# Performance work log

Hardware: AMD Instinct MI355X
Metric: run time of the kernel (lower is better)

Reference implementation:

```python
import jax, jax.numpy as jnp
import numpy as np

NUM_ENT = 14541
NUM_REL = 474
D = 400
B = 32
N_CAND = 14505


def setup_inputs() -> dict:
    key = jax.random.key(0)
    k0, k1, k2, k4, k5 = jax.random.split(key, 5)
    return {
        "arg0_1": jax.random.normal(k0, (NUM_ENT, D), dtype=jnp.float32),   # entity embeddings
        "arg1_1": jax.random.normal(k1, (NUM_REL, D), dtype=jnp.float32),   # relation centers
        "arg2_1": jax.random.uniform(k2, (NUM_REL, D), dtype=jnp.float32),  # relation offsets (box widths)
        "arg3_1": jnp.ones((1,), dtype=jnp.float32),                        # margin gamma
        "arg4_1": jax.random.randint(k4, (B, 2), 0, NUM_REL),               # (head_id, rel_id) pairs
        "arg5_1": jax.random.randint(k5, (4, N_CAND), 0, NUM_ENT),          # candidate entity ids (row 0 used)
    }


def reference(arg0_1, arg1_1, arg2_1, arg3_1, arg4_1, arg5_1):
    # Gather heads / relation params
    head = arg0_1[arg4_1[:, 0]]            # [B, D]
    rel_c = arg1_1[arg4_1[:, 1]]           # [B, D]
    rel_o = arg2_1[arg4_1[:, 1]]           # [B, D]

    query = (head + rel_c)[:, None, :]     # [B, 1, D] box center
    offset = rel_o[:, None, :]             # [B, 1, D] box width

    # Candidate tail embeddings: only row 0 of arg5_1 is used in the graph
    cand = arg0_1[arg5_1[0].reshape(-1)][None, :, :]  # [1, N_CAND, D]

    d = jnp.abs(cand - query)                           # [B, N_CAND, D]
    dist_outside = jax.nn.relu(d - offset).sum(-1)      # [B, N_CAND]
    dist_inside = jnp.abs(jnp.minimum(d, offset)).sum(-1)

    return arg3_1 - dist_outside - 0.02 * dist_inside   # [B, N_CAND]
```

## Files before the change

kernel.cpp:

```cpp
#include <hip/hip_runtime.h>

#define DIM     400
#define NENT    14541
#define B       32
#define NCAND   14505
#define NROUND  3627
#define NSTRIPS 256
#define THREADS 256
#define DROWS   14508
#define CVTN    (DROWS * 50)
#define CVTBLK  ((CVTN + THREADS - 1) / THREADS)

typedef __attribute__((ext_vector_type(2))) _Float16 half2_t;

static __device__ __forceinline__ half2_t bch(unsigned u) {
    return __builtin_bit_cast(half2_t, u);
}
static __device__ __forceinline__ half2_t habs2(half2_t x) {
    unsigned u = __builtin_bit_cast(unsigned, x) & 0x7fff7fffu;
    return __builtin_bit_cast(half2_t, u);
}
static __device__ __forceinline__ unsigned pkh(float x, float y) {
    half2_t h;
    h.x = (_Float16)x;
    h.y = (_Float16)y;
    return __builtin_bit_cast(unsigned, h);
}
static __device__ __forceinline__ float dot2acc(half2_t m, float s) {
#if __has_builtin(__builtin_amdgcn_fdot2)
    const half2_t ones = {(_Float16)1.f, (_Float16)1.f};
    return __builtin_amdgcn_fdot2(m, ones, s, false);
#else
    return s + (float)m.x + (float)m.y;
#endif
}

__global__ void setup_kernel(const float* __restrict__ ent,
                             const float* __restrict__ relc,
                             const float* __restrict__ relo,
                             const float* __restrict__ onev,
                             const int*   __restrict__ pairs,
                             const int*   __restrict__ cidx,
                             uint4* __restrict__ dense16,
                             _Float16* __restrict__ q16,
                             _Float16* __restrict__ o16,
                             float* __restrict__ baseg) {
    const int blk = blockIdx.x;
    const int tid = threadIdx.x;
    if (blk < CVTBLK) {
        int i = blk * THREADS + tid;
        if (i >= CVTN) return;
        int row = i / 50;
        int col = i - row * 50;
        int n  = row < NCAND ? row : NCAND - 1;
        int ci = cidx[n];
        const float4* s4 = (const float4*)(ent + (size_t)ci * DIM) + col * 2;
        float4 a = s4[0], c = s4[1];
        uint4 d;
        d.x = pkh(a.x, a.y);
        d.y = pkh(a.z, a.w);
        d.z = pkh(c.x, c.y);
        d.w = pkh(c.z, c.w);
        dense16[i] = d;
    } else {
        const int b = blk - CVTBLK;
        const int h = pairs[2 * b + 0];
        const int r = pairs[2 * b + 1];
        float so = 0.f;
        for (int i = tid; i < DIM; i += THREADS) {
            float qv = ent[(size_t)h * DIM + i] + relc[(size_t)r * DIM + i];
            float ov = relo[(size_t)r * DIM + i];
            q16[(size_t)b * DIM + i] = (_Float16)qv;
            o16[(size_t)b * DIM + i] = (_Float16)(0.98f * ov);
            so += ov;
        }
        __shared__ float sred[4];
        for (int off = 32; off; off >>= 1) so += __shfl_down(so, off);
        if ((tid & 63) == 0) sred[tid >> 6] = so;
        __syncthreads();
        if (tid == 0)
            baseg[b] = onev[0] + 0.98f * (sred[0] + sred[1] + sred[2] + sred[3]);
    }
}

__global__ __launch_bounds__(THREADS, 2)
void score_f16(const uint4* __restrict__ dense16,
               const uint4* __restrict__ q16,
               const uint4* __restrict__ o16,
               const float* __restrict__ baseg,
               float* __restrict__ out) {
    const int fid  = blockIdx.x;
    const int xcd  = fid & 7;
    const int rest = fid >> 3;
    const int beta = rest & 3;
    const int tc   = rest >> 2;
    const int strip = xcd + 8 * tc;

    const int r0 = strip * 14 + (strip < 43 ? strip : 43);
    const int r1 = r0 + 14 + (strip < 43 ? 1 : 0);

    const int tid  = threadIdx.x;
    const int wid  = tid >> 6;
    const int lane = tid & 63;
    const int u    = lane & 15;
    const int g    = lane >> 4;
    const int b0   = __builtin_amdgcn_readfirstlane(8 * beta + 2 * wid);
    const int b1   = b0 + 1;

    const uint4* qa = q16 + (size_t)b0 * 50;
    const uint4* oa = o16 + (size_t)b0 * 50;
    const uint4* qc = q16 + (size_t)b1 * 50;
    const uint4* oc = o16 + (size_t)b1 * 50;

    uint4 q0[4], o0[4], q1[4], o1[4];
    q0[0] = qa[u]; q0[1] = qa[u + 16]; q0[2] = qa[u + 32];
    o0[0] = oa[u]; o0[1] = oa[u + 16]; o0[2] = oa[u + 32];
    q1[0] = qc[u]; q1[1] = qc[u + 16]; q1[2] = qc[u + 32];
    o1[0] = oc[u]; o1[1] = oc[u + 16]; o1[2] = oc[u + 32];
    q0[3] = q0[0]; o0[3] = o0[0]; q1[3] = q1[0]; o1[3] = o1[0];
    if (u < 2) {
        q0[3] = qa[48 + u]; o0[3] = oa[48 + u];
        q1[3] = qc[48 + u]; o1[3] = oc[48 + u];
    }
    const float base0 = baseg[b0];
    const float base1 = baseg[b1];

    const half2_t K002 = {(_Float16)0.02f, (_Float16)0.02f};

#define PAIR(cu, qu, ou, SS)                                    \
    {                                                           \
        half2_t cc_ = bch(cu), qq_ = bch(qu), oo_ = bch(ou);    \
        half2_t dd_ = cc_ - qq_;                                \
        half2_t aa_ = habs2(dd_);                               \
        half2_t ee_ = aa_ * K002 + oo_;                         \
        half2_t mm_ = __builtin_elementwise_max(aa_, ee_);      \
        SS = dot2acc(mm_, SS);                                  \
    }
#define PROC(C, Q, O, SA, SB)                                   \
    PAIR(C.x, Q.x, O.x, SA) PAIR(C.y, Q.y, O.y, SB)             \
    PAIR(C.z, Q.z, O.z, SA) PAIR(C.w, Q.w, O.w, SB)

    for (int rr = r0; rr < r1; rr += 2) {
        const int rA = rr;
        const int rB = (rr + 1 < r1) ? rr + 1 : rr;
        const uint4* pA = dense16 + (size_t)(4 * rA + g) * 50;
        const uint4* pB = dense16 + (size_t)(4 * rB + g) * 50;

        uint4 av0 = pA[u], av1 = pA[u + 16], av2 = pA[u + 32];
        uint4 bv0 = pB[u], bv1 = pB[u + 16], bv2 = pB[u + 32];
        uint4 av3, bv3;
        if (u < 2) { av3 = pA[48 + u]; bv3 = pB[48 + u]; }

        float sA00 = 0.f, sA01 = 0.f, sA10 = 0.f, sA11 = 0.f;
        float sB00 = 0.f, sB01 = 0.f, sB10 = 0.f, sB11 = 0.f;

        PROC(av0, q0[0], o0[0], sA00, sA01)
        PROC(av1, q0[1], o0[1], sA00, sA01)
        PROC(av2, q0[2], o0[2], sA00, sA01)
        PROC(av0, q1[0], o1[0], sA10, sA11)
        PROC(av1, q1[1], o1[1], sA10, sA11)
        PROC(av2, q1[2], o1[2], sA10, sA11)
        if (u < 2) {
            PROC(av3, q0[3], o0[3], sA00, sA01)
            PROC(av3, q1[3], o1[3], sA10, sA11)
        }
        PROC(bv0, q0[0], o0[0], sB00, sB01)
        PROC(bv1, q0[1], o0[1], sB00, sB01)
        PROC(bv2, q0[2], o0[2], sB00, sB01)
        PROC(bv0, q1[0], o1[0], sB10, sB11)
        PROC(bv1, q1[1], o1[1], sB10, sB11)
        PROC(bv2, q1[2], o1[2], sB10, sB11)
        if (u < 2) {
            PROC(bv3, q0[3], o0[3], sB00, sB01)
            PROC(bv3, q1[3], o1[3], sB10, sB11)
        }

        float sA0 = sA00 + sA01;
        float sA1 = sA10 + sA11;
        float sB0 = sB00 + sB01;
        float sB1 = sB10 + sB11;
        sA0 += __shfl_xor(sA0, 1); sA1 += __shfl_xor(sA1, 1);
        sB0 += __shfl_xor(sB0, 1); sB1 += __shfl_xor(sB1, 1);
        sA0 += __shfl_xor(sA0, 2); sA1 += __shfl_xor(sA1, 2);
        sB0 += __shfl_xor(sB0, 2); sB1 += __shfl_xor(sB1, 2);
        sA0 += __shfl_xor(sA0, 4); sA1 += __shfl_xor(sA1, 4);
        sB0 += __shfl_xor(sB0, 4); sB1 += __shfl_xor(sB1, 4);
        sA0 += __shfl_xor(sA0, 8); sA1 += __shfl_xor(sA1, 8);
        sB0 += __shfl_xor(sB0, 8); sB1 += __shfl_xor(sB1, 8);

        if (u == 0) {
            const int candA = 4 * rA + g;
            const int candB = 4 * rB + g;
            if (candA < NCAND) {
                out[(size_t)b0 * NCAND + candA] = base0 - sA0;
                out[(size_t)b1 * NCAND + candA] = base1 - sA1;
            }
            if (rB != rA && candB < NCAND) {
                out[(size_t)b0 * NCAND + candB] = base0 - sB0;
                out[(size_t)b1 * NCAND + candB] = base1 - sB1;
            }
        }
    }
#undef PROC
#undef PAIR
}

__global__ __launch_bounds__(THREADS, 2)
void score_f32(const float* __restrict__ ent,
               const float* __restrict__ relc,
               const float* __restrict__ relo,
               const float* __restrict__ onev,
               const int*   __restrict__ pairs,
               const int*   __restrict__ cidx,
               float* __restrict__ out) {
    const int fid  = blockIdx.x;
    const int xcd  = fid & 7;
    const int rest = fid >> 3;
    const int bq   = rest & 7;
    const int tc   = rest >> 3;
    const int t    = xcd + 8 * tc;

    const int tid  = threadIdx.x;
    const int lane = tid & 63;
    const int u    = lane & 15;
    const int g    = lane >> 4;
    const int b    = __builtin_amdgcn_readfirstlane(bq * 4 + (tid >> 6));

    const int hd = pairs[b * 2 + 0];
    const int rl = pairs[b * 2 + 1];
    const float4* hb = (const float4*)(ent  + (size_t)hd * DIM) + u;
    const float4* cb = (const float4*)(relc + (size_t)rl * DIM) + u;
    const float4* ob = (const float4*)(relo + (size_t)rl * DIM) + u;

    float4 q[7], o[7];
    float oa = 0.f;
#pragma unroll
    for (int k = 0; k < 6; ++k) {
        float4 h = hb[16 * k], c = cb[16 * k];
        q[k] = make_float4(h.x + c.x, h.y + c.y, h.z + c.z, h.w + c.w);
        o[k] = ob[16 * k];
        oa += o[k].x + o[k].y + o[k].z + o[k].w;
    }
    if (u < 4) {
        float4 h = hb[96], c = cb[96];
        q[6] = make_float4(h.x + c.x, h.y + c.y, h.z + c.z, h.w + c.w);
        o[6] = ob[96];
        oa += o[6].x + o[6].y + o[6].z + o[6].w;
    }
    oa += __shfl_xor(oa, 1);
    oa += __shfl_xor(oa, 2);
    oa += __shfl_xor(oa, 4);
    oa += __shfl_xor(oa, 8);
    const float base = onev[0] + 0.98f * oa;

    const float4* entu = (const float4*)ent + u;

#define E(vc, vq, vo, AM, AD)                     \
        {                                         \
            float d_ = (vc) - (vq);               \
            AM += fmaxf(fabsf(d_), (vo));         \
            AD += fabsf(d_);                      \
        }
#define F4(k, AM, AD)                             \
        E(cbuf[k].x, q[k].x, o[k].x, AM, AD)      \
        E(cbuf[k].y, q[k].y, o[k].y, AM, AD)      \
        E(cbuf[k].z, q[k].z, o[k].z, AM, AD)      \
        E(cbuf[k].w, q[k].w, o[k].w, AM, AD)

    for (int rr = t; rr < NROUND; rr += NSTRIPS) {
        const int cand = 4 * rr + g;
        const int ci   = cidx[cand < NCAND ? cand : NCAND - 1];
        const float4* p = entu + (size_t)ci * 100;

        float4 cbuf[7];
#pragma unroll
        for (int k = 0; k < 6; ++k) cbuf[k] = p[16 * k];
        if (u < 4) cbuf[6] = p[96];

        float am0 = 0.f, ad0 = 0.f, am1 = 0.f, ad1 = 0.f;
        F4(0, am0, ad0) F4(1, am1, ad1)
        F4(2, am0, ad0) F4(3, am1, ad1)
        F4(4, am0, ad0) F4(5, am1, ad1)
        if (u < 4) { F4(6, am0, ad0) }

        float s_ = fmaf(-0.98f, am0 + am1, -0.02f * (ad0 + ad1));
        s_ += __shfl_xor(s_, 1);
        s_ += __shfl_xor(s_, 2);
        s_ += __shfl_xor(s_, 4);
        s_ += __shfl_xor(s_, 8);

        if (u == 0 && cand < NCAND)
            out[(size_t)b * NCAND + cand] = base + s_;
    }
#undef F4
#undef E
}

extern "C" void kernel_launch(void* const* d_in, const int* in_sizes, int n_in,
                              void* d_out, int out_size, void* d_ws, size_t ws_size,
                              hipStream_t stream) {
    const float* ent   = (const float*)d_in[0];
    const float* relc  = (const float*)d_in[1];
    const float* relo  = (const float*)d_in[2];
    const float* onev  = (const float*)d_in[3];
    const int*   pairs = (const int*)d_in[4];
    const int*   cidx  = (const int*)d_in[5];
    float*       out   = (float*)d_out;

    const size_t denB = (size_t)DROWS * DIM * 2;
    const size_t qB   = (size_t)B * DIM * 2;
    const size_t need = denB + 2 * qB + B * sizeof(float);

    if (ws_size >= need) {
        unsigned char* w = (unsigned char*)d_ws;
        uint4*    dense16 = (uint4*)w;
        _Float16* q16     = (_Float16*)(w + denB);
        _Float16* o16     = (_Float16*)(w + denB + qB);
        float*    baseg   = (float*)(w + denB + 2 * qB);

        setup_kernel<<<CVTBLK + B, THREADS, 0, stream>>>(
            ent, relc, relo, onev, pairs, cidx, dense16, q16, o16, baseg);
        score_f16<<<8 * 4 * 32, THREADS, 0, stream>>>(
            dense16, (const uint4*)q16, (const uint4*)o16, baseg, out);
    } else {
        score_f32<<<8 * 8 * 32, THREADS, 0, stream>>>(
            ent, relc, relo, onev, pairs, cidx, out);
    }
}
```

Baseline: 39.84 us.

## Compute query/offset in score kernel and assign one batch row per wave

```diff
diff --git a/kernel.cpp b/kernel.cpp
--- a/kernel.cpp
+++ b/kernel.cpp
@@ -5,7 +5,6 @@
 #define B       32
 #define NCAND   14505
 #define NROUND  3627
-#define NSTRIPS 256
 #define THREADS 256
 #define DROWS   14508
 #define CVTN    (DROWS * 50)
@@ -36,64 +35,37 @@
 }
 
 __global__ void setup_kernel(const float* __restrict__ ent,
-                             const float* __restrict__ relc,
-                             const float* __restrict__ relo,
-                             const float* __restrict__ onev,
-                             const int*   __restrict__ pairs,
                              const int*   __restrict__ cidx,
-                             uint4* __restrict__ dense16,
-                             _Float16* __restrict__ q16,
-                             _Float16* __restrict__ o16,
-                             float* __restrict__ baseg) {
-    const int blk = blockIdx.x;
-    const int tid = threadIdx.x;
-    if (blk < CVTBLK) {
-        int i = blk * THREADS + tid;
-        if (i >= CVTN) return;
-        int row = i / 50;
-        int col = i - row * 50;
-        int n  = row < NCAND ? row : NCAND - 1;
-        int ci = cidx[n];
-        const float4* s4 = (const float4*)(ent + (size_t)ci * DIM) + col * 2;
-        float4 a = s4[0], c = s4[1];
-        uint4 d;
-        d.x = pkh(a.x, a.y);
-        d.y = pkh(a.z, a.w);
-        d.z = pkh(c.x, c.y);
-        d.w = pkh(c.z, c.w);
-        dense16[i] = d;
-    } else {
-        const int b = blk - CVTBLK;
-        const int h = pairs[2 * b + 0];
-        const int r = pairs[2 * b + 1];
-        float so = 0.f;
-        for (int i = tid; i < DIM; i += THREADS) {
-            float qv = ent[(size_t)h * DIM + i] + relc[(size_t)r * DIM + i];
-            float ov = relo[(size_t)r * DIM + i];
-            q16[(size_t)b * DIM + i] = (_Float16)qv;
-            o16[(size_t)b * DIM + i] = (_Float16)(0.98f * ov);
-            so += ov;
-        }
-        __shared__ float sred[4];
-        for (int off = 32; off; off >>= 1) so += __shfl_down(so, off);
-        if ((tid & 63) == 0) sred[tid >> 6] = so;
-        __syncthreads();
-        if (tid == 0)
-            baseg[b] = onev[0] + 0.98f * (sred[0] + sred[1] + sred[2] + sred[3]);
-    }
+                             uint4* __restrict__ dense16) {
+    int i = blockIdx.x * THREADS + threadIdx.x;
+    if (i >= CVTN) return;
+    int row = i / 50;
+    int col = i - row * 50;
+    int n  = row < NCAND ? row : NCAND - 1;
+    int ci = cidx[n];
+    const float4* s4 = (const float4*)(ent + (size_t)ci * DIM) + col * 2;
+    float4 a = s4[0], c = s4[1];
+    uint4 d;
+    d.x = pkh(a.x, a.y);
+    d.y = pkh(a.z, a.w);
+    d.z = pkh(c.x, c.y);
+    d.w = pkh(c.z, c.w);
+    dense16[i] = d;
 }
 
 __global__ __launch_bounds__(THREADS, 2)
 void score_f16(const uint4* __restrict__ dense16,
-               const uint4* __restrict__ q16,
-               const uint4* __restrict__ o16,
-               const float* __restrict__ baseg,
+               const float* __restrict__ ent,
+               const float* __restrict__ relc,
+               const float* __restrict__ relo,
+               const float* __restrict__ onev,
+               const int*   __restrict__ pairs,
                float* __restrict__ out) {
     const int fid  = blockIdx.x;
     const int xcd  = fid & 7;
     const int rest = fid >> 3;
-    const int beta = rest & 3;
-    const int tc   = rest >> 2;
+    const int bq   = rest & 7;
+    const int tc   = rest >> 3;
     const int strip = xcd + 8 * tc;
 
     const int r0 = strip * 14 + (strip < 43 ? strip : 43);
@@ -104,26 +76,53 @@
     const int lane = tid & 63;
     const int u    = lane & 15;
     const int g    = lane >> 4;
-    const int b0   = __builtin_amdgcn_readfirstlane(8 * beta + 2 * wid);
-    const int b1   = b0 + 1;
-
-    const uint4* qa = q16 + (size_t)b0 * 50;
-    const uint4* oa = o16 + (size_t)b0 * 50;
-    const uint4* qc = q16 + (size_t)b1 * 50;
-    const uint4* oc = o16 + (size_t)b1 * 50;
-
-    uint4 q0[4], o0[4], q1[4], o1[4];
-    q0[0] = qa[u]; q0[1] = qa[u + 16]; q0[2] = qa[u + 32];
-    o0[0] = oa[u]; o0[1] = oa[u + 16]; o0[2] = oa[u + 32];
-    q1[0] = qc[u]; q1[1] = qc[u + 16]; q1[2] = qc[u + 32];
-    o1[0] = oc[u]; o1[1] = oc[u + 16]; o1[2] = oc[u + 32];
-    q0[3] = q0[0]; o0[3] = o0[0]; q1[3] = q1[0]; o1[3] = o1[0];
+    const int b    = __builtin_amdgcn_readfirstlane(4 * bq + wid);
+
+    const int hd = pairs[2 * b + 0];
+    const int rl = pairs[2 * b + 1];
+    const float4* hp = (const float4*)(ent  + (size_t)hd * DIM);
+    const float4* cp = (const float4*)(relc + (size_t)rl * DIM);
+    const float4* op = (const float4*)(relo + (size_t)rl * DIM);
+
+    uint4 q[4], o[4];
+    float oa = 0.f;
+#pragma unroll
+    for (int k = 0; k < 3; ++k) {
+        const int f = 2 * u + 32 * k;
+        float4 h0 = hp[f], h1 = hp[f + 1];
+        float4 c0 = cp[f], c1 = cp[f + 1];
+        float4 v0 = op[f], v1 = op[f + 1];
+        q[k].x = pkh(h0.x + c0.x, h0.y + c0.y);
+        q[k].y = pkh(h0.z + c0.z, h0.w + c0.w);
+        q[k].z = pkh(h1.x + c1.x, h1.y + c1.y);
+        q[k].w = pkh(h1.z + c1.z, h1.w + c1.w);
+        o[k].x = pkh(0.98f * v0.x, 0.98f * v0.y);
+        o[k].y = pkh(0.98f * v0.z, 0.98f * v0.w);
+        o[k].z = pkh(0.98f * v1.x, 0.98f * v1.y);
+        o[k].w = pkh(0.98f * v1.z, 0.98f * v1.w);
+        oa += v0.x + v0.y + v0.z + v0.w + v1.x + v1.y + v1.z + v1.w;
+    }
+    q[3] = q[0]; o[3] = o[0];
     if (u < 2) {
-        q0[3] = qa[48 + u]; o0[3] = oa[48 + u];
-        q1[3] = qc[48 + u]; o1[3] = oc[48 + u];
-    }
-    const float base0 = baseg[b0];
-    const float base1 = baseg[b1];
+        const int f = 96 + 2 * u;
+        float4 h0 = hp[f], h1 = hp[f + 1];
+        float4 c0 = cp[f], c1 = cp[f + 1];
+        float4 v0 = op[f], v1 = op[f + 1];
+        q[3].x = pkh(h0.x + c0.x, h0.y + c0.y);
+        q[3].y = pkh(h0.z + c0.z, h0.w + c0.w);
+        q[3].z = pkh(h1.x + c1.x, h1.y + c1.y);
+        q[3].w = pkh(h1.z + c1.z, h1.w + c1.w);
+        o[3].x = pkh(0.98f * v0.x, 0.98f * v0.y);
+        o[3].y = pkh(0.98f * v0.z, 0.98f * v0.w);
+        o[3].z = pkh(0.98f * v1.x, 0.98f * v1.y);
+        o[3].w = pkh(0.98f * v1.z, 0.98f * v1.w);
+        oa += v0.x + v0.y + v0.z + v0.w + v1.x + v1.y + v1.z + v1.w;
+    }
+    oa += __shfl_xor(oa, 1);
+    oa += __shfl_xor(oa, 2);
+    oa += __shfl_xor(oa, 4);
+    oa += __shfl_xor(oa, 8);
+    const float base = onev[0] + 0.98f * oa;
 
     const half2_t K002 = {(_Float16)0.02f, (_Float16)0.02f};
 
@@ -151,54 +150,30 @@
         uint4 av3, bv3;
         if (u < 2) { av3 = pA[48 + u]; bv3 = pB[48 + u]; }
 
-        float sA00 = 0.f, sA01 = 0.f, sA10 = 0.f, sA11 = 0.f;
-        float sB00 = 0.f, sB01 = 0.f, sB10 = 0.f, sB11 = 0.f;
-
-        PROC(av0, q0[0], o0[0], sA00, sA01)
-        PROC(av1, q0[1], o0[1], sA00, sA01)
-        PROC(av2, q0[2], o0[2], sA00, sA01)
-        PROC(av0, q1[0], o1[0], sA10, sA11)
-        PROC(av1, q1[1], o1[1], sA10, sA11)
-        PROC(av2, q1[2], o1[2], sA10, sA11)
-        if (u < 2) {
-            PROC(av3, q0[3], o0[3], sA00, sA01)
-            PROC(av3, q1[3], o1[3], sA10, sA11)
-        }
-        PROC(bv0, q0[0], o0[0], sB00, sB01)
-        PROC(bv1, q0[1], o0[1], sB00, sB01)
-        PROC(bv2, q0[2], o0[2], sB00, sB01)
-        PROC(bv0, q1[0], o1[0], sB10, sB11)
-        PROC(bv1, q1[1], o1[1], sB10, sB11)
-        PROC(bv2, q1[2], o1[2], sB10, sB11)
-        if (u < 2) {
-            PROC(bv3, q0[3], o0[3], sB00, sB01)
-            PROC(bv3, q1[3], o1[3], sB10, sB11)
-        }
-
-        float sA0 = sA00 + sA01;
-        float sA1 = sA10 + sA11;
-        float sB0 = sB00 + sB01;
-        float sB1 = sB10 + sB11;
-        sA0 += __shfl_xor(sA0, 1); sA1 += __shfl_xor(sA1, 1);
-        sB0 += __shfl_xor(sB0, 1); sB1 += __shfl_xor(sB1, 1);
-        sA0 += __shfl_xor(sA0, 2); sA1 += __shfl_xor(sA1, 2);
-        sB0 += __shfl_xor(sB0, 2); sB1 += __shfl_xor(sB1, 2);
-        sA0 += __shfl_xor(sA0, 4); sA1 += __shfl_xor(sA1, 4);
-        sB0 += __shfl_xor(sB0, 4); sB1 += __shfl_xor(sB1, 4);
-        sA0 += __shfl_xor(sA0, 8); sA1 += __shfl_xor(sA1, 8);
-        sB0 += __shfl_xor(sB0, 8); sB1 += __shfl_xor(sB1, 8);
+        float sA0 = 0.f, sA1 = 0.f, sB0 = 0.f, sB1 = 0.f;
+        PROC(av0, q[0], o[0], sA0, sA1)
+        PROC(av1, q[1], o[1], sA0, sA1)
+        PROC(av2, q[2], o[2], sA0, sA1)
+        if (u < 2) { PROC(av3, q[3], o[3], sA0, sA1) }
+        PROC(bv0, q[0], o[0], sB0, sB1)
+        PROC(bv1, q[1], o[1], sB0, sB1)
+        PROC(bv2, q[2], o[2], sB0, sB1)
+        if (u < 2) { PROC(bv3, q[3], o[3], sB0, sB1) }
+
+        float sA = sA0 + sA1;
+        float sB = sB0 + sB1;
+        sA += __shfl_xor(sA, 1); sB += __shfl_xor(sB, 1);
+        sA += __shfl_xor(sA, 2); sB += __shfl_xor(sB, 2);
+        sA += __shfl_xor(sA, 4); sB += __shfl_xor(sB, 4);
+        sA += __shfl_xor(sA, 8); sB += __shfl_xor(sB, 8);
 
         if (u == 0) {
             const int candA = 4 * rA + g;
             const int candB = 4 * rB + g;
-            if (candA < NCAND) {
-                out[(size_t)b0 * NCAND + candA] = base0 - sA0;
-                out[(size_t)b1 * NCAND + candA] = base1 - sA1;
-            }
-            if (rB != rA && candB < NCAND) {
-                out[(size_t)b0 * NCAND + candB] = base0 - sB0;
-                out[(size_t)b1 * NCAND + candB] = base1 - sB1;
-            }
+            if (candA < NCAND)
+                out[(size_t)b * NCAND + candA] = base - sA;
+            if (rB != rA && candB < NCAND)
+                out[(size_t)b * NCAND + candB] = base - sB;
         }
     }
 #undef PROC
@@ -267,7 +242,7 @@
         E(cbuf[k].z, q[k].z, o[k].z, AM, AD)      \
         E(cbuf[k].w, q[k].w, o[k].w, AM, AD)
 
-    for (int rr = t; rr < NROUND; rr += NSTRIPS) {
+    for (int rr = t; rr < NROUND; rr += 256) {
         const int cand = 4 * rr + g;
         const int ci   = cidx[cand < NCAND ? cand : NCAND - 1];
         const float4* p = entu + (size_t)ci * 100;
@@ -308,20 +283,12 @@
     float*       out   = (float*)d_out;
 
     const size_t denB = (size_t)DROWS * DIM * 2;
-    const size_t qB   = (size_t)B * DIM * 2;
-    const size_t need = denB + 2 * qB + B * sizeof(float);
-
-    if (ws_size >= need) {
-        unsigned char* w = (unsigned char*)d_ws;
-        uint4*    dense16 = (uint4*)w;
-        _Float16* q16     = (_Float16*)(w + denB);
-        _Float16* o16     = (_Float16*)(w + denB + qB);
-        float*    baseg   = (float*)(w + denB + 2 * qB);
-
-        setup_kernel<<<CVTBLK + B, THREADS, 0, stream>>>(
-            ent, relc, relo, onev, pairs, cidx, dense16, q16, o16, baseg);
-        score_f16<<<8 * 4 * 32, THREADS, 0, stream>>>(
-            dense16, (const uint4*)q16, (const uint4*)o16, baseg, out);
+
+    if (ws_size >= denB) {
+        uint4* dense16 = (uint4*)d_ws;
+        setup_kernel<<<CVTBLK, THREADS, 0, stream>>>(ent, cidx, dense16);
+        score_f16<<<8 * 8 * 32, THREADS, 0, stream>>>(
+            dense16, ent, relc, relo, onev, pairs, out);
     } else {
         score_f32<<<8 * 8 * 32, THREADS, 0, stream>>>(
             ent, relc, relo, onev, pairs, cidx, out);
```

Measured after the change: 42.02 us. +5.5%, slower.

## Remap f16 scoring to one query per wave with three candidates per iteration

Applied to the files above, without the earlier changes.

```diff
diff --git a/kernel.cpp b/kernel.cpp
--- a/kernel.cpp
+++ b/kernel.cpp
@@ -4,12 +4,11 @@
 #define NENT    14541
 #define B       32
 #define NCAND   14505
-#define NROUND  3627
-#define NSTRIPS 256
+#define NSTRIP  303
+#define DROWS   14544
+#define CVTN    (DROWS * 50)
+#define CVTBLK  ((CVTN + 255) / 256)
 #define THREADS 256
-#define DROWS   14508
-#define CVTN    (DROWS * 50)
-#define CVTBLK  ((CVTN + THREADS - 1) / THREADS)
 
 typedef __attribute__((ext_vector_type(2))) _Float16 half2_t;
 
@@ -92,38 +91,29 @@
     const int fid  = blockIdx.x;
     const int xcd  = fid & 7;
     const int rest = fid >> 3;
-    const int beta = rest & 3;
-    const int tc   = rest >> 2;
+    const int bq   = rest & 7;
+    const int tc   = rest >> 3;
     const int strip = xcd + 8 * tc;
-
-    const int r0 = strip * 14 + (strip < 43 ? strip : 43);
-    const int r1 = r0 + 14 + (strip < 43 ? 1 : 0);
+    if (strip >= NSTRIP) return;
+
+    const int r0 = strip * 12;
+    const int r1 = r0 + 12;
 
     const int tid  = threadIdx.x;
     const int wid  = tid >> 6;
     const int lane = tid & 63;
     const int u    = lane & 15;
     const int g    = lane >> 4;
-    const int b0   = __builtin_amdgcn_readfirstlane(8 * beta + 2 * wid);
-    const int b1   = b0 + 1;
-
-    const uint4* qa = q16 + (size_t)b0 * 50;
-    const uint4* oa = o16 + (size_t)b0 * 50;
-    const uint4* qc = q16 + (size_t)b1 * 50;
-    const uint4* oc = o16 + (size_t)b1 * 50;
-
-    uint4 q0[4], o0[4], q1[4], o1[4];
-    q0[0] = qa[u]; q0[1] = qa[u + 16]; q0[2] = qa[u + 32];
-    o0[0] = oa[u]; o0[1] = oa[u + 16]; o0[2] = oa[u + 32];
-    q1[0] = qc[u]; q1[1] = qc[u + 16]; q1[2] = qc[u + 32];
-    o1[0] = oc[u]; o1[1] = oc[u + 16]; o1[2] = oc[u + 32];
-    q0[3] = q0[0]; o0[3] = o0[0]; q1[3] = q1[0]; o1[3] = o1[0];
-    if (u < 2) {
-        q0[3] = qa[48 + u]; o0[3] = oa[48 + u];
-        q1[3] = qc[48 + u]; o1[3] = oc[48 + u];
-    }
-    const float base0 = baseg[b0];
-    const float base1 = baseg[b1];
+    const int b    = __builtin_amdgcn_readfirstlane(4 * bq + wid);
+
+    const uint4* qa = q16 + (size_t)b * 50;
+    const uint4* oa = o16 + (size_t)b * 50;
+    uint4 q[4], o[4];
+    q[0] = qa[u]; q[1] = qa[u + 16]; q[2] = qa[u + 32];
+    o[0] = oa[u]; o[1] = oa[u + 16]; o[2] = oa[u + 32];
+    q[3] = q[0]; o[3] = o[0];
+    if (u < 2) { q[3] = qa[48 + u]; o[3] = oa[48 + u]; }
+    const float base = baseg[b];
 
     const half2_t K002 = {(_Float16)0.02f, (_Float16)0.02f};
 
@@ -140,65 +130,44 @@
     PAIR(C.x, Q.x, O.x, SA) PAIR(C.y, Q.y, O.y, SB)             \
     PAIR(C.z, Q.z, O.z, SA) PAIR(C.w, Q.w, O.w, SB)
 
-    for (int rr = r0; rr < r1; rr += 2) {
-        const int rA = rr;
-        const int rB = (rr + 1 < r1) ? rr + 1 : rr;
-        const uint4* pA = dense16 + (size_t)(4 * rA + g) * 50;
-        const uint4* pB = dense16 + (size_t)(4 * rB + g) * 50;
+    for (int rr = r0; rr < r1; rr += 3) {
+        const uint4* pA = dense16 + (size_t)(4 * rr + g) * 50;
+        const uint4* pB = pA + 200;
+        const uint4* pC = pA + 400;
 
         uint4 av0 = pA[u], av1 = pA[u + 16], av2 = pA[u + 32];
         uint4 bv0 = pB[u], bv1 = pB[u + 16], bv2 = pB[u + 32];
-        uint4 av3, bv3;
-        if (u < 2) { av3 = pA[48 + u]; bv3 = pB[48 + u]; }
-
-        float sA00 = 0.f, sA01 = 0.f, sA10 = 0.f, sA11 = 0.f;
-        float sB00 = 0.f, sB01 = 0.f, sB10 = 0.f, sB11 = 0.f;
-
-        PROC(av0, q0[0], o0[0], sA00, sA01)
-        PROC(av1, q0[1], o0[1], sA00, sA01)
-        PROC(av2, q0[2], o0[2], sA00, sA01)
-        PROC(av0, q1[0], o1[0], sA10, sA11)
-        PROC(av1, q1[1], o1[1], sA10, sA11)
-        PROC(av2, q1[2], o1[2], sA10, sA11)
-        if (u < 2) {
-            PROC(av3, q0[3], o0[3], sA00, sA01)
-            PROC(av3, q1[3], o1[3], sA10, sA11)
-        }
-        PROC(bv0, q0[0], o0[0], sB00, sB01)
-        PROC(bv1, q0[1], o0[1], sB00, sB01)
-        PROC(bv2, q0[2], o0[2], sB00, sB01)
-        PROC(bv0, q1[0], o1[0], sB10, sB11)
-        PROC(bv1, q1[1], o1[1], sB10, sB11)
-        PROC(bv2, q1[2], o1[2], sB10, sB11)
-        if (u < 2) {
-            PROC(bv3, q0[3], o0[3], sB00, sB01)
-            PROC(bv3, q1[3], o1[3], sB10, sB11)
-        }
-
-        float sA0 = sA00 + sA01;
-        float sA1 = sA10 + sA11;
-        float sB0 = sB00 + sB01;
-        float sB1 = sB10 + sB11;
-        sA0 += __shfl_xor(sA0, 1); sA1 += __shfl_xor(sA1, 1);
-        sB0 += __shfl_xor(sB0, 1); sB1 += __shfl_xor(sB1, 1);
-        sA0 += __shfl_xor(sA0, 2); sA1 += __shfl_xor(sA1, 2);
-        sB0 += __shfl_xor(sB0, 2); sB1 += __shfl_xor(sB1, 2);
-        sA0 += __shfl_xor(sA0, 4); sA1 += __shfl_xor(sA1, 4);
-        sB0 += __shfl_xor(sB0, 4); sB1 += __shfl_xor(sB1, 4);
-        sA0 += __shfl_xor(sA0, 8); sA1 += __shfl_xor(sA1, 8);
-        sB0 += __shfl_xor(sB0, 8); sB1 += __shfl_xor(sB1, 8);
+        uint4 cv0 = pC[u], cv1 = pC[u + 16], cv2 = pC[u + 32];
+        uint4 av3, bv3, cv3;
+        if (u < 2) { av3 = pA[48 + u]; bv3 = pB[48 + u]; cv3 = pC[48 + u]; }
+
+        float sA0 = 0.f, sA1 = 0.f, sB0 = 0.f, sB1 = 0.f, sC0 = 0.f, sC1 = 0.f;
+        PROC(av0, q[0], o[0], sA0, sA1)
+        PROC(av1, q[1], o[1], sA0, sA1)
+        PROC(av2, q[2], o[2], sA0, sA1)
+        if (u < 2) { PROC(av3, q[3], o[3], sA0, sA1) }
+        PROC(bv0, q[0], o[0], sB0, sB1)
+        PROC(bv1, q[1], o[1], sB0, sB1)
+        PROC(bv2, q[2], o[2], sB0, sB1)
+        if (u < 2) { PROC(bv3, q[3], o[3], sB0, sB1) }
+        PROC(cv0, q[0], o[0], sC0, sC1)
+        PROC(cv1, q[1], o[1], sC0, sC1)
+        PROC(cv2, q[2], o[2], sC0, sC1)
+        if (u < 2) { PROC(cv3, q[3], o[3], sC0, sC1) }
+
+        float sA = sA0 + sA1;
+        float sB = sB0 + sB1;
+        float sC = sC0 + sC1;
+        sA += __shfl_xor(sA, 1); sB += __shfl_xor(sB, 1); sC += __shfl_xor(sC, 1);
+        sA += __shfl_xor(sA, 2); sB += __shfl_xor(sB, 2); sC += __shfl_xor(sC, 2);
+        sA += __shfl_xor(sA, 4); sB += __shfl_xor(sB, 4); sC += __shfl_xor(sC, 4);
+        sA += __shfl_xor(sA, 8); sB += __shfl_xor(sB, 8); sC += __shfl_xor(sC, 8);
 
         if (u == 0) {
-            const int candA = 4 * rA + g;
-            const int candB = 4 * rB + g;
-            if (candA < NCAND) {
-                out[(size_t)b0 * NCAND + candA] = base0 - sA0;
-                out[(size_t)b1 * NCAND + candA] = base1 - sA1;
-            }
-            if (rB != rA && candB < NCAND) {
-                out[(size_t)b0 * NCAND + candB] = base0 - sB0;
-                out[(size_t)b1 * NCAND + candB] = base1 - sB1;
-            }
+            const int candA = 4 * rr + g;
+            if (candA < NCAND)     out[(size_t)b * NCAND + candA]     = base - sA;
+            if (candA + 4 < NCAND) out[(size_t)b * NCAND + candA + 4] = base - sB;
+            if (candA + 8 < NCAND) out[(size_t)b * NCAND + candA + 8] = base - sC;
         }
     }
 #undef PROC
@@ -267,7 +236,7 @@
         E(cbuf[k].z, q[k].z, o[k].z, AM, AD)      \
         E(cbuf[k].w, q[k].w, o[k].w, AM, AD)
 
-    for (int rr = t; rr < NROUND; rr += NSTRIPS) {
+    for (int rr = t; rr < 3627; rr += 256) {
         const int cand = 4 * rr + g;
         const int ci   = cidx[cand < NCAND ? cand : NCAND - 1];
         const float4* p = entu + (size_t)ci * 100;
@@ -320,7 +289,7 @@
 
         setup_kernel<<<CVTBLK + B, THREADS, 0, stream>>>(
             ent, relc, relo, onev, pairs, cidx, dense16, q16, o16, baseg);
-        score_f16<<<8 * 4 * 32, THREADS, 0, stream>>>(
+        score_f16<<<8 * 8 * 38, THREADS, 0, stream>>>(
             dense16, (const uint4*)q16, (const uint4*)o16, baseg, out);
     } else {
         score_f32<<<8 * 8 * 32, THREADS, 0, stream>>>(
```

New measurement: 39.84 us. No clear change (+0.0%).
